# Performance work log

Measured on AMD Instinct MI355X. Metric: run time of the kernel, lower is better.

Reference implementation:

```python
import jax, jax.numpy as jnp
import numpy as np

D = 1024; H = 16; DH = 64; L = 24; S = 4096; DFF = 4096
QB = 7; NC = 2 ** QB; TOPK = 10; EOS = NC + 1
SCALE = float(1.0 / np.sqrt(DH))


def _ln(x, g):
    m = jnp.mean(x, axis=-1, keepdims=True)
    v = jnp.var(x, axis=-1, keepdims=True)
    return (x - m) * jax.lax.rsqrt(v + 1e-5) * g


def _mlp(h, w1, b1, w2, b2, w3, b3):
    h = jax.nn.relu(h @ w1 + b1)
    h = jax.nn.relu(h @ w2 + b2)
    return h @ w3 + b3


def _decode(x, k_cache, v_cache, ln1_g, Wq, Wk, Wv, Wo, ln2_g, Wg, Wu, Wd, lnf_g):
    # single-token decode through L pre-norm layers with KV cache
    def step(h, xs):
        l1, wq, wk, wv, wo, l2, wg, wu, wd, K, V = xs
        hn = _ln(h, l1)
        q = (hn @ wq).reshape(H, DH)
        kn = (hn @ wk).reshape(1, H, DH)
        vn = (hn @ wv).reshape(1, H, DH)
        Kf = jnp.concatenate([K, kn], axis=0)  # [S+1,H,DH]
        Vf = jnp.concatenate([V, vn], axis=0)
        att = jax.nn.softmax(jnp.einsum('hd,shd->hs', q, Kf) * SCALE, axis=-1)
        o = jnp.einsum('hs,shd->hd', att, Vf).reshape(D)
        h = h + o @ wo
        hn = _ln(h, l2)
        h = h + (jax.nn.gelu(hn @ wg) * (hn @ wu)) @ wd  # GLU FF
        return h, None

    res, _ = jax.lax.scan(step, x, (ln1_g, Wq, Wk, Wv, Wo, ln2_g, Wg, Wu, Wd, k_cache, v_cache))
    return _ln(res, lnf_g)


def setup_inputs() -> dict:
    key = jax.random.key(0)
    ks = jax.random.split(key, 40)
    def r(i, shape, s=0.02):
        return jax.random.normal(ks[i], shape, dtype=jnp.float32) * s
    inp = {
        'x': r(0, (D,), 1.0),
        'k_cache': r(1, (L, S, H, DH), 1.0),
        'v_cache': r(2, (L, S, H, DH), 1.0),
        'ln1_g': jnp.ones((L, D), jnp.float32),
        'Wq': r(3, (L, D, D)), 'Wk': r(4, (L, D, D)), 'Wv': r(5, (L, D, D)), 'Wo': r(6, (L, D, D)),
        'ln2_g': jnp.ones((L, D), jnp.float32),
        'Wg': r(7, (L, D, DFF)), 'Wu': r(8, (L, D, DFF)), 'Wd': r(9, (L, DFF, D)),
        'lnf_g': jnp.ones((D,), jnp.float32),
        'h1_w1': r(10, (D, D)), 'h1_b1': jnp.zeros((D,), jnp.float32),
        'h1_w2': r(11, (D, D)), 'h1_b2': jnp.zeros((D,), jnp.float32),
        'h1_w3': r(12, (D, NC + 2)), 'h1_b3': jnp.zeros((NC + 2,), jnp.float32),
        'h2_w1': r(13, (2 * D, D)), 'h2_b1': jnp.zeros((D,), jnp.float32),
        'h2_w2': r(14, (D, D)), 'h2_b2': jnp.zeros((D,), jnp.float32),
        'h2_w3': r(15, (D, NC)), 'h2_b3': jnp.zeros((NC,), jnp.float32),
        'h3_w1': r(16, (3 * D, D)), 'h3_b1': jnp.zeros((D,), jnp.float32),
        'h3_w2': r(17, (D, D)), 'h3_b2': jnp.zeros((D,), jnp.float32),
        'h3_w3': r(18, (D, NC)), 'h3_b3': jnp.zeros((NC,), jnp.float32),
        'c1_emb': r(19, (NC, D), 1.0),
        'c2_emb': r(20, (NC, D), 1.0),
    }
    return inp


def reference(x, k_cache, v_cache, ln1_g, Wq, Wk, Wv, Wo, ln2_g, Wg, Wu, Wd, lnf_g,
              h1_w1, h1_b1, h1_w2, h1_b2, h1_w3, h1_b3,
              h2_w1, h2_b1, h2_w2, h2_b2, h2_w3, h2_b3,
              h3_w1, h3_b1, h3_w2, h3_b2, h3_w3, h3_b3,
              c1_emb, c2_emb):
    res = _decode(x, k_cache, v_cache, ln1_g, Wq, Wk, Wv, Wo, ln2_g, Wg, Wu, Wd, lnf_g)

    k1, k2, k3 = jax.random.split(jax.random.key(42), 3)

    # stage 1: z coordinate (quantized) with EOS-masked top-k sampling
    logits_z = _mlp(res, h1_w1, h1_b1, h1_w2, h1_b2, h1_w3, h1_b3)  # [NC+2]
    tpz, tiz = jax.lax.top_k(jax.nn.softmax(logits_z), TOPK)
    is_eos = tiz[0] == EOS
    mp = tpz * (tiz != EOS).astype(tpz.dtype)
    mp = mp / mp.sum()
    z = jnp.where(is_eos, EOS, tiz[jax.random.categorical(k1, jnp.log(mp + 1e-9))])
    emb_z = c1_emb[jnp.minimum(z, NC - 1)]

    # stage 2: y coordinate
    logits_y = _mlp(jnp.concatenate([res, emb_z]), h2_w1, h2_b1, h2_w2, h2_b2, h2_w3, h2_b3)
    tpy, tiy = jax.lax.top_k(jax.nn.softmax(logits_y), TOPK)
    y = tiy[jax.random.categorical(k2, jnp.log(tpy + 1e-9))]
    emb_y = c2_emb[y]

    # stage 3: x coordinate
    logits_x = _mlp(jnp.concatenate([res, emb_z, emb_y]), h3_w1, h3_b1, h3_w2, h3_b2, h3_w3, h3_b3)
    tpx, tix = jax.lax.top_k(jax.nn.softmax(logits_x), TOPK)
    xc = tix[jax.random.categorical(k3, jnp.log(tpx + 1e-9))]

    xyz = jnp.stack([xc, y, z])
    logits_cat = jnp.concatenate([logits_z, logits_y, logits_x])  # [130+128+128]=386
    return xyz, logits_cat
```

## Files before the change

kernel.cpp:

```cpp
#include <hip/hip_runtime.h>
#include <cstdint>
#include <cstring>
#include <cmath>

constexpr int kH    = 16;
constexpr int kL    = 24;
constexpr int kS    = 4096;
constexpr int kEOS  = 129;
constexpr float kSCALE = 0.125f;
constexpr int kNS   = 32;
constexpr int kTOK  = kS / kNS;

struct G10 { float g[10]; };


__device__ __forceinline__ float wave_sum(float v) {
  v += __shfl_xor(v, 32, 64); v += __shfl_xor(v, 16, 64);
  v += __shfl_xor(v, 8, 64);  v += __shfl_xor(v, 4, 64);
  v += __shfl_xor(v, 2, 64);  v += __shfl_xor(v, 1, 64);
  return v;
}
__device__ __forceinline__ float wave_max(float v) {
  v = fmaxf(v, __shfl_xor(v, 32, 64)); v = fmaxf(v, __shfl_xor(v, 16, 64));
  v = fmaxf(v, __shfl_xor(v, 8, 64));  v = fmaxf(v, __shfl_xor(v, 4, 64));
  v = fmaxf(v, __shfl_xor(v, 2, 64));  v = fmaxf(v, __shfl_xor(v, 1, 64));
  return v;
}
__device__ __forceinline__ float block_sum4(float v, float* red) {
  v = wave_sum(v);
  if ((threadIdx.x & 63) == 0) red[threadIdx.x >> 6] = v;
  __syncthreads();
  float s = red[0] + red[1] + red[2] + red[3];
  __syncthreads();
  return s;
}
__device__ __forceinline__ float block_max4(float v, float* red) {
  v = wave_max(v);
  if ((threadIdx.x & 63) == 0) red[threadIdx.x >> 6] = v;
  __syncthreads();
  float s = fmaxf(fmaxf(red[0], red[1]), fmaxf(red[2], red[3]));
  __syncthreads();
  return s;
}

__device__ __forceinline__ void ln_stats(const float* __restrict__ h, float* red,
                                         float& mean, float& rs) {
  int tid = threadIdx.x;
  float v0 = h[tid], v1 = h[tid + 256], v2 = h[tid + 512], v3 = h[tid + 768];
  float s = block_sum4(v0 + v1 + v2 + v3, red);
  mean = s * (1.0f / 1024.0f);
  float d0 = v0 - mean, d1 = v1 - mean, d2 = v2 - mean, d3 = v3 - mean;
  float sq = block_sum4(d0 * d0 + d1 * d1 + d2 * d2 + d3 * d3, red);
  rs = 1.0f / sqrtf(sq * (1.0f / 1024.0f) + 1e-5f);
}

__device__ __forceinline__ float gelu_f(float x) {
  float t = tanhf(0.7978845608028654f * (x + 0.044715f * x * x * x));
  return 0.5f * x * (1.0f + t);
}


__global__ __launch_bounds__(256) void k_ln_qkv(const float* __restrict__ h,
                                                const float* __restrict__ g,
                                                const float* __restrict__ Wq,
                                                const float* __restrict__ Wk,
                                                const float* __restrict__ Wv,
                                                float* __restrict__ qkv_part,
                                                float* __restrict__ hres) {
  __shared__ float red4[4];
  __shared__ float xs[64];
  __shared__ float4 sh4[256];
  int tid = threadIdx.x;
  float mean, rs;
  ln_stats(h, red4, mean, rs);
  int by = blockIdx.y, rb = by * 64;
  if (tid < 64) xs[tid] = (h[rb + tid] - mean) * rs * g[rb + tid];
  if (blockIdx.x == 0 && tid < 64) hres[rb + tid] = h[rb + tid];
  __syncthreads();
  int c4 = tid & 63, w = tid >> 6;
  int vcol4 = blockIdx.x * 64 + c4;
  int mat = vcol4 >> 8;
  const float* W = (mat == 0) ? Wq : ((mat == 1) ? Wk : Wv);
  const float4* W4 = reinterpret_cast<const float4*>(W);
  int wcol4 = vcol4 & 255;
  float4 acc = {0.f, 0.f, 0.f, 0.f};
  int r0 = w * 16;
  #pragma unroll
  for (int i = 0; i < 16; ++i) {
    int j = r0 + i;
    float xv = xs[j];
    float4 wv = W4[(size_t)(rb + j) * 256 + wcol4];
    acc.x += xv * wv.x; acc.y += xv * wv.y; acc.z += xv * wv.z; acc.w += xv * wv.w;
  }
  sh4[tid] = acc;
  __syncthreads();
  if (tid < 64) {
    float4 a = sh4[tid], b = sh4[tid + 64], c = sh4[tid + 128], d = sh4[tid + 192];
    a.x += b.x + c.x + d.x; a.y += b.y + c.y + d.y;
    a.z += b.z + c.z + d.z; a.w += b.w + c.w + d.w;
    reinterpret_cast<float4*>(qkv_part)[(size_t)by * 768 + blockIdx.x * 64 + tid] = a;
  }
}

__global__ __launch_bounds__(256) void k_attn(const float* __restrict__ qkv_part,
                                              const float* __restrict__ Kc,
                                              const float* __restrict__ Vc,
                                              float* __restrict__ part) {
  __shared__ float4 q4[16];
  __shared__ float4 kn4[16];
  __shared__ float4 vn4[16];
  __shared__ float sc[132];
  __shared__ float red4[4];
  __shared__ float4 ored[16][17];
  int split = blockIdx.x, head = blockIdx.y;
  int tid = threadIdx.x;
  if (tid < 64) {
    float s = 0.f;
    #pragma unroll
    for (int p = 0; p < 16; ++p) s += qkv_part[p * 3072 + head * 64 + tid];
    ((float*)q4)[tid] = s;
  } else if (tid < 128) {
    int d = tid - 64; float s = 0.f;
    #pragma unroll
    for (int p = 0; p < 16; ++p) s += qkv_part[p * 3072 + 1024 + head * 64 + d];
    ((float*)kn4)[d] = s;
  } else if (tid < 192) {
    int d = tid - 128; float s = 0.f;
    #pragma unroll
    for (int p = 0; p < 16; ++p) s += qkv_part[p * 3072 + 2048 + head * 64 + d];
    ((float*)vn4)[d] = s;
  }
  __syncthreads();
  int base = split * kTOK;
  bool last = (split == kNS - 1);
  int count = kTOK + (last ? 1 : 0);
  int wv = tid >> 6, lane = tid & 63, grp = lane >> 4, l16 = lane & 15;
  int g0 = wv * 4 + grp;
  float4 qf = q4[l16];
  const float4* K4 = reinterpret_cast<const float4*>(Kc);
  const float4* V4 = reinterpret_cast<const float4*>(Vc);
  #pragma unroll
  for (int i = 0; i < 8; ++i) {
    int t = g0 + 16 * i;
    float4 kf = K4[(size_t)(base + t) * 256 + head * 16 + l16];
    float d = qf.x * kf.x + qf.y * kf.y + qf.z * kf.z + qf.w * kf.w;
    d += __shfl_xor(d, 1, 16); d += __shfl_xor(d, 2, 16);
    d += __shfl_xor(d, 4, 16); d += __shfl_xor(d, 8, 16);
    if (l16 == 0) sc[t] = d * kSCALE;
  }
  if (last && g0 == 0) {
    float4 kf = kn4[l16];
    float d = qf.x * kf.x + qf.y * kf.y + qf.z * kf.z + qf.w * kf.w;
    d += __shfl_xor(d, 1, 16); d += __shfl_xor(d, 2, 16);
    d += __shfl_xor(d, 4, 16); d += __shfl_xor(d, 8, 16);
    if (l16 == 0) sc[128] = d * kSCALE;
  }
  float4 vreg[8];
  #pragma unroll
  for (int i = 0; i < 8; ++i) {
    int t = g0 + 16 * i;
    vreg[i] = V4[(size_t)(base + t) * 256 + head * 16 + l16];
  }
  __syncthreads();
  float v = (tid < count) ? sc[tid] : -1e30f;
  float m = block_max4(v, red4);
  float pexp = 0.f;
  if (tid < count) { pexp = expf(sc[tid] - m); sc[tid] = pexp; }
  float l = block_sum4(pexp, red4);
  float4 acc = {0.f, 0.f, 0.f, 0.f};
  #pragma unroll
  for (int i = 0; i < 8; ++i) {
    int t = g0 + 16 * i;
    float p = sc[t];
    acc.x += p * vreg[i].x; acc.y += p * vreg[i].y;
    acc.z += p * vreg[i].z; acc.w += p * vreg[i].w;
  }
  if (last && g0 == 0) {
    float p = sc[128];
    float4 vf = vn4[l16];
    acc.x += p * vf.x; acc.y += p * vf.y; acc.z += p * vf.z; acc.w += p * vf.w;
  }
  ored[g0][l16] = acc;
  __syncthreads();
  float* pp = &part[(size_t)(head * kNS + split) * 68];
  if (tid < 16) {
    float4 s = ored[0][tid];
    #pragma unroll
    for (int k = 1; k < 16; ++k) {
      float4 b = ored[k][tid];
      s.x += b.x; s.y += b.y; s.z += b.z; s.w += b.w;
    }
    reinterpret_cast<float4*>(pp + 4)[tid] = s;
  }
  if (tid == 0) { pp[0] = m; pp[1] = l; }
}

__global__ __launch_bounds__(256) void k_comb_wo(const float* __restrict__ part,
                                                 const float* __restrict__ Wo,
                                                 float* __restrict__ hout) {
  __shared__ float o[64];
  __shared__ float4 sh4[256];
  int tid = threadIdx.x;
  int head = blockIdx.y, bx = blockIdx.x;
  if (tid < 64) {
    const float* pp = part + (size_t)(head * kNS) * 68;
    float m = -1e30f;
    for (int s = 0; s < kNS; ++s) m = fmaxf(m, pp[s * 68]);
    float l = 0.f, acc = 0.f;
    for (int s = 0; s < kNS; ++s) {
      float e = expf(pp[s * 68] - m);
      l += e * pp[s * 68 + 1];
      acc += e * pp[s * 68 + 4 + tid];
    }
    o[tid] = acc / l;
  }
  __syncthreads();
  int c4 = tid & 15, w = tid >> 4;
  int vcol4 = bx * 16 + c4;
  const float4* W4 = reinterpret_cast<const float4*>(Wo);
  float4 acc = {0.f, 0.f, 0.f, 0.f};
  int r0 = w * 4;
  #pragma unroll
  for (int i = 0; i < 4; ++i) {
    int r = r0 + i;
    float xv = o[r];
    float4 wv = W4[(size_t)(head * 64 + r) * 256 + vcol4];
    acc.x += xv * wv.x; acc.y += xv * wv.y; acc.z += xv * wv.z; acc.w += xv * wv.w;
  }
  sh4[tid] = acc;
  __syncthreads();
  if (tid < 16) {
    float4 a = sh4[tid];
    #pragma unroll
    for (int k = 1; k < 16; ++k) {
      float4 b = sh4[k * 16 + tid];
      a.x += b.x; a.y += b.y; a.z += b.z; a.w += b.w;
    }
    int vcol = (bx * 16 + tid) * 4;
    atomicAdd(&hout[vcol],     a.x);
    atomicAdd(&hout[vcol + 1], a.y);
    atomicAdd(&hout[vcol + 2], a.z);
    atomicAdd(&hout[vcol + 3], a.w);
  }
}

__global__ __launch_bounds__(256) void k_ln_gu(const float* __restrict__ h,
                                               const float* __restrict__ g,
                                               const float* __restrict__ Wg,
                                               const float* __restrict__ Wu,
                                               float* __restrict__ gu_part,
                                               float* __restrict__ hres) {
  __shared__ float red4[4];
  __shared__ float xs[64];
  __shared__ float4 sh4[256];
  int tid = threadIdx.x;
  float mean, rs;
  ln_stats(h, red4, mean, rs);
  int by = blockIdx.y, rb = by * 64;
  if (tid < 64) xs[tid] = (h[rb + tid] - mean) * rs * g[rb + tid];
  if (blockIdx.x == 0 && tid < 64) hres[rb + tid] = h[rb + tid];
  __syncthreads();
  int c4 = tid & 63, w = tid >> 6;
  int vcol4 = blockIdx.x * 64 + c4;
  int mat = vcol4 >> 10;
  const float4* W4 = reinterpret_cast<const float4*>(mat ? Wu : Wg);
  int wcol4 = vcol4 & 1023;
  float4 acc = {0.f, 0.f, 0.f, 0.f};
  int r0 = w * 16;
  #pragma unroll
  for (int i = 0; i < 16; ++i) {
    int j = r0 + i;
    float xv = xs[j];
    float4 wv = W4[(size_t)(rb + j) * 1024 + wcol4];
    acc.x += xv * wv.x; acc.y += xv * wv.y; acc.z += xv * wv.z; acc.w += xv * wv.w;
  }
  sh4[tid] = acc;
  __syncthreads();
  if (tid < 64) {
    float4 a = sh4[tid], b = sh4[tid + 64], c = sh4[tid + 128], d = sh4[tid + 192];
    a.x += b.x + c.x + d.x; a.y += b.y + c.y + d.y;
    a.z += b.z + c.z + d.z; a.w += b.w + c.w + d.w;
    reinterpret_cast<float4*>(gu_part)[(size_t)by * 2048 + blockIdx.x * 64 + tid] = a;
  }
}

__global__ __launch_bounds__(256) void k_act_wd(const float* __restrict__ gu_part,
                                                const float* __restrict__ Wd,
                                                float* __restrict__ hout) {
  __shared__ float xs[64];
  __shared__ float4 sh4[256];
  int tid = threadIdx.x;
  int by = blockIdx.y, rb = by * 64;
  if (tid < 64) {
    float gs = 0.f, us = 0.f;
    #pragma unroll
    for (int p = 0; p < 16; ++p) {
      gs += gu_part[p * 8192 + rb + tid];
      us += gu_part[p * 8192 + 4096 + rb + tid];
    }
    xs[tid] = gelu_f(gs) * us;
  }
  __syncthreads();
  int c4 = tid & 63, w = tid >> 6;
  int vcol4 = blockIdx.x * 64 + c4;
  const float4* W4 = reinterpret_cast<const float4*>(Wd);
  float4 acc = {0.f, 0.f, 0.f, 0.f};
  int r0 = w * 16;
  #pragma unroll
  for (int i = 0; i < 16; ++i) {
    int j = r0 + i;
    float xv = xs[j];
    float4 wv = W4[(size_t)(rb + j) * 256 + vcol4];
    acc.x += xv * wv.x; acc.y += xv * wv.y; acc.z += xv * wv.z; acc.w += xv * wv.w;
  }
  sh4[tid] = acc;
  __syncthreads();
  if (tid < 64) {
    float4 a = sh4[tid], b = sh4[tid + 64], c = sh4[tid + 128], d = sh4[tid + 192];
    a.x += b.x + c.x + d.x; a.y += b.y + c.y + d.y;
    a.z += b.z + c.z + d.z; a.w += b.w + c.w + d.w;
    int vcol = (blockIdx.x * 64 + tid) * 4;
    atomicAdd(&hout[vcol],     a.x);
    atomicAdd(&hout[vcol + 1], a.y);
    atomicAdd(&hout[vcol + 2], a.z);
    atomicAdd(&hout[vcol + 3], a.w);
  }
}


__global__ __launch_bounds__(256) void k_head_g1(const float* __restrict__ hA,
                                                 const float* __restrict__ lnfg,
                                                 const float* __restrict__ catE,
                                                 const float* __restrict__ W,
                                                 float* __restrict__ t1_part,
                                                 const float* __restrict__ b3,
                                                 float* __restrict__ logits, int n3) {
  __shared__ float red4[4];
  __shared__ float xs[64];
  __shared__ float4 sh4[256];
  int tid = threadIdx.x;
  float mean, rs;
  ln_stats(hA, red4, mean, rs);
  int by = blockIdx.y, rb = by * 64;
  if (blockIdx.x == 0 && by == 0 && tid < n3) logits[tid] = b3[tid];
  if (tid < 64) {
    int r = rb + tid;
    xs[tid] = (r < 1024) ? (hA[r] - mean) * rs * lnfg[r] : catE[r - 1024];
  }
  __syncthreads();
  int c4 = tid & 15, w = tid >> 4;
  int vcol4 = blockIdx.x * 16 + c4;
  const float4* W4 = reinterpret_cast<const float4*>(W);
  float4 acc = {0.f, 0.f, 0.f, 0.f};
  int r0 = w * 4;
  #pragma unroll
  for (int i = 0; i < 4; ++i) {
    float xv = xs[r0 + i];
    float4 wv = W4[(size_t)(rb + r0 + i) * 256 + vcol4];
    acc.x += xv * wv.x; acc.y += xv * wv.y; acc.z += xv * wv.z; acc.w += xv * wv.w;
  }
  sh4[tid] = acc;
  __syncthreads();
  if (tid < 16) {
    float4 a = sh4[tid];
    #pragma unroll
    for (int k = 1; k < 16; ++k) {
      float4 b = sh4[k * 16 + tid];
      a.x += b.x; a.y += b.y; a.z += b.z; a.w += b.w;
    }
    reinterpret_cast<float4*>(t1_part)[(size_t)by * 256 + blockIdx.x * 16 + tid] = a;
  }
}

__global__ __launch_bounds__(256) void k_head_g2(const float* __restrict__ t1_part,
                                                 int ny,
                                                 const float* __restrict__ b1,
                                                 const float* __restrict__ W,
                                                 float* __restrict__ t2_part) {
  __shared__ float xs[64];
  __shared__ float4 sh4[256];
  int tid = threadIdx.x;
  int by = blockIdx.y, rb = by * 64;
  if (tid < 64) {
    float s = b1[rb + tid];
    for (int p = 0; p < ny; ++p) s += t1_part[p * 1024 + rb + tid];
    xs[tid] = fmaxf(s, 0.f);
  }
  __syncthreads();
  int c4 = tid & 15, w = tid >> 4;
  int vcol4 = blockIdx.x * 16 + c4;
  const float4* W4 = reinterpret_cast<const float4*>(W);
  float4 acc = {0.f, 0.f, 0.f, 0.f};
  int r0 = w * 4;
  #pragma unroll
  for (int i = 0; i < 4; ++i) {
    float xv = xs[r0 + i];
    float4 wv = W4[(size_t)(rb + r0 + i) * 256 + vcol4];
    acc.x += xv * wv.x; acc.y += xv * wv.y; acc.z += xv * wv.z; acc.w += xv * wv.w;
  }
  sh4[tid] = acc;
  __syncthreads();
  if (tid < 16) {
    float4 a = sh4[tid];
    #pragma unroll
    for (int k = 1; k < 16; ++k) {
      float4 b = sh4[k * 16 + tid];
      a.x += b.x; a.y += b.y; a.z += b.z; a.w += b.w;
    }
    reinterpret_cast<float4*>(t2_part)[(size_t)by * 256 + blockIdx.x * 16 + tid] = a;
  }
}

__global__ __launch_bounds__(256) void k_head_g3(const float* __restrict__ t2_part,
                                                 const float* __restrict__ b2,
                                                 const float* __restrict__ W,
                                                 float* __restrict__ logits, int n3) {
  __shared__ float xs[64];
  int tid = threadIdx.x;
  int rb = blockIdx.x * 64;
  if (tid < 64) {
    float s = b2[rb + tid];
    #pragma unroll
    for (int p = 0; p < 16; ++p) s += t2_part[p * 1024 + rb + tid];
    xs[tid] = fmaxf(s, 0.f);
  }
  __syncthreads();
  if (tid < n3) {
    float acc = 0.f;
    for (int i = 0; i < 64; ++i) acc += xs[i] * W[(size_t)(rb + i) * n3 + tid];
    atomicAdd(&logits[tid], acc);
  }
}


__global__ void k_sample1(const float* __restrict__ logits,
                          const float* __restrict__ c1_emb,
                          float* __restrict__ embdst,
                          float* __restrict__ out_xyz,
                          G10 gb) {
  __shared__ int zsh;
  int tid = threadIdx.x;
  if (tid == 0) {
    float p[130];
    float mx = -1e30f;
    for (int i = 0; i < 130; ++i) mx = fmaxf(mx, logits[i]);
    float s = 0.f;
    for (int i = 0; i < 130; ++i) { p[i] = expf(logits[i] - mx); s += p[i]; }
    for (int i = 0; i < 130; ++i) p[i] /= s;
    float tp[10]; int ti[10];
    for (int k = 0; k < 10; ++k) {
      float best = -1.f; int bi = 0;
      for (int i = 0; i < 130; ++i)
        if (p[i] > best) { best = p[i]; bi = i; }
      tp[k] = best; ti[k] = bi; p[bi] = -2.f;
    }
    int is_eos = (ti[0] == kEOS);
    float mp[10]; float ssum = 0.f;
    for (int k = 0; k < 10; ++k) {
      mp[k] = tp[k] * ((ti[k] != kEOS) ? 1.f : 0.f);
      ssum += mp[k];
    }
    float bestsc = -1e30f; int ba = 0;
    for (int k = 0; k < 10; ++k) {
      float sc = logf(mp[k] / ssum + 1e-9f) + gb.g[k];
      if (sc > bestsc) { bestsc = sc; ba = k; }
    }
    int z = is_eos ? kEOS : ti[ba];
    zsh = z;
    out_xyz[2] = (float)z;
  }
  __syncthreads();
  int zi = zsh; if (zi > 127) zi = 127;
  for (int i = tid; i < 1024; i += blockDim.x)
    embdst[i] = c1_emb[(size_t)zi * 1024 + i];
}

__global__ void k_sample23(const float* __restrict__ logits,
                           const float* __restrict__ emb,
                           float* __restrict__ embdst,
                           float* __restrict__ outslot,
                           G10 gb) {
  __shared__ int ysh;
  int tid = threadIdx.x;
  if (tid == 0) {
    float p[128];
    float mx = -1e30f;
    for (int i = 0; i < 128; ++i) mx = fmaxf(mx, logits[i]);
    float s = 0.f;
    for (int i = 0; i < 128; ++i) { p[i] = expf(logits[i] - mx); s += p[i]; }
    for (int i = 0; i < 128; ++i) p[i] /= s;
    float tp[10]; int ti[10];
    for (int k = 0; k < 10; ++k) {
      float best = -1.f; int bi = 0;
      for (int i = 0; i < 128; ++i)
        if (p[i] > best) { best = p[i]; bi = i; }
      tp[k] = best; ti[k] = bi; p[bi] = -2.f;
    }
    float bestsc = -1e30f; int ba = 0;
    for (int k = 0; k < 10; ++k) {
      float sc = logf(tp[k] + 1e-9f) + gb.g[k];
      if (sc > bestsc) { bestsc = sc; ba = k; }
    }
    int y = ti[ba];
    ysh = y;
    *outslot = (float)y;
  }
  __syncthreads();
  if (emb != nullptr) {
    int y = ysh;
    for (int i = tid; i < 1024; i += blockDim.x)
      embdst[i] = emb[(size_t)y * 1024 + i];
  }
}


static inline uint32_t rotl32(uint32_t x, uint32_t r) { return (x << r) | (x >> (32 - r)); }

static void threefry2x32(uint32_t k0, uint32_t k1, uint32_t x0, uint32_t x1,
                         uint32_t* o0, uint32_t* o1) {
  uint32_t ks0 = k0, ks1 = k1, ks2 = k0 ^ k1 ^ 0x1BD11BDAu;
  const uint32_t R0[4] = {13, 15, 26, 6};
  const uint32_t R1[4] = {17, 29, 16, 24};
  x0 += ks0; x1 += ks1;
  for (int j = 0; j < 4; ++j) { x0 += x1; x1 = rotl32(x1, R0[j]); x1 ^= x0; }
  x0 += ks1; x1 += ks2 + 1u;
  for (int j = 0; j < 4; ++j) { x0 += x1; x1 = rotl32(x1, R1[j]); x1 ^= x0; }
  x0 += ks2; x1 += ks0 + 2u;
  for (int j = 0; j < 4; ++j) { x0 += x1; x1 = rotl32(x1, R0[j]); x1 ^= x0; }
  x0 += ks0; x1 += ks1 + 3u;
  for (int j = 0; j < 4; ++j) { x0 += x1; x1 = rotl32(x1, R1[j]); x1 ^= x0; }
  x0 += ks1; x1 += ks2 + 4u;
  for (int j = 0; j < 4; ++j) { x0 += x1; x1 = rotl32(x1, R0[j]); x1 ^= x0; }
  x0 += ks2; x1 += ks0 + 5u;
  *o0 = x0; *o1 = x1;
}

static void gumbel10_part(uint32_t k0, uint32_t k1, float* g) {
  const float tiny = 1.1754943508222875e-38f;
  for (int i = 0; i < 10; ++i) {
    uint32_t a, c;
    threefry2x32(k0, k1, 0u, (uint32_t)i, &a, &c);
    uint32_t bits = a ^ c;
    uint32_t fb = (bits >> 9) | 0x3f800000u;
    float f; memcpy(&f, &fb, 4);
    f -= 1.0f;
    float u = f * (1.0f - tiny) + tiny;
    if (u < tiny) u = tiny;
    g[i] = -logf(-logf(u));
  }
}


extern "C" void kernel_launch(void* const* d_in, const int* in_sizes, int n_in,
                              void* d_out, int out_size, void* d_ws, size_t ws_size,
                              hipStream_t stream) {
  (void)in_sizes; (void)n_in; (void)out_size; (void)ws_size;
  const float* x      = (const float*)d_in[0];
  const float* kcache = (const float*)d_in[1];
  const float* vcache = (const float*)d_in[2];
  const float* ln1g   = (const float*)d_in[3];
  const float* Wq     = (const float*)d_in[4];
  const float* Wk     = (const float*)d_in[5];
  const float* Wv     = (const float*)d_in[6];
  const float* Wo     = (const float*)d_in[7];
  const float* ln2g   = (const float*)d_in[8];
  const float* Wg     = (const float*)d_in[9];
  const float* Wu     = (const float*)d_in[10];
  const float* Wd     = (const float*)d_in[11];
  const float* lnfg   = (const float*)d_in[12];
  const float* h1w1 = (const float*)d_in[13]; const float* h1b1 = (const float*)d_in[14];
  const float* h1w2 = (const float*)d_in[15]; const float* h1b2 = (const float*)d_in[16];
  const float* h1w3 = (const float*)d_in[17]; const float* h1b3 = (const float*)d_in[18];
  const float* h2w1 = (const float*)d_in[19]; const float* h2b1 = (const float*)d_in[20];
  const float* h2w2 = (const float*)d_in[21]; const float* h2b2 = (const float*)d_in[22];
  const float* h2w3 = (const float*)d_in[23]; const float* h2b3 = (const float*)d_in[24];
  const float* h3w1 = (const float*)d_in[25]; const float* h3b1 = (const float*)d_in[26];
  const float* h3w2 = (const float*)d_in[27]; const float* h3b2 = (const float*)d_in[28];
  const float* h3w3 = (const float*)d_in[29]; const float* h3b3 = (const float*)d_in[30];
  const float* c1emb = (const float*)d_in[31];
  const float* c2emb = (const float*)d_in[32];

  float* ws = (float*)d_ws;
  float* hA   = ws;
  float* hB   = ws + 1024;
  float* qkvp = ws + 2048;
  float* part = ws + 51200;
  float* gup  = ws + 86016;
  float* catE = ws + 217088;
  float* t2p  = ws + 219136;
  float* t1p  = gup;
  float* out  = (float*)d_out;

  for (int l = 0; l < kL; ++l) {
    const float* Wq_l = Wq + (size_t)l * 1024 * 1024;
    const float* Wk_l = Wk + (size_t)l * 1024 * 1024;
    const float* Wv_l = Wv + (size_t)l * 1024 * 1024;
    const float* Wo_l = Wo + (size_t)l * 1024 * 1024;
    const float* Wg_l = Wg + (size_t)l * 1024 * 4096;
    const float* Wu_l = Wu + (size_t)l * 1024 * 4096;
    const float* Wd_l = Wd + (size_t)l * 4096 * 1024;
    const float* Kc_l = kcache + (size_t)l * kS * 1024;
    const float* Vc_l = vcache + (size_t)l * kS * 1024;
    const float* h_in = (l == 0) ? x : hA;

    k_ln_qkv<<<dim3(12, 16), 256, 0, stream>>>(h_in, ln1g + (size_t)l * 1024,
                                               Wq_l, Wk_l, Wv_l, qkvp, hB);
    k_attn<<<dim3(kNS, kH), 256, 0, stream>>>(qkvp, Kc_l, Vc_l, part);
    k_comb_wo<<<dim3(16, kH), 256, 0, stream>>>(part, Wo_l, hB);
    k_ln_gu<<<dim3(32, 16), 256, 0, stream>>>(hB, ln2g + (size_t)l * 1024,
                                              Wg_l, Wu_l, gup, hA);
    k_act_wd<<<dim3(4, 64), 256, 0, stream>>>(gup, Wd_l, hA);
  }

  uint32_t k1a, k1b, k2a, k2b, k3a, k3b;
  threefry2x32(0u, 42u, 0u, 0u, &k1a, &k1b);
  threefry2x32(0u, 42u, 0u, 1u, &k2a, &k2b);
  threefry2x32(0u, 42u, 0u, 2u, &k3a, &k3b);
  G10 G1, G2, G3;
  gumbel10_part(k1a, k1b, G1.g);
  gumbel10_part(k2a, k2b, G2.g);
  gumbel10_part(k3a, k3b, G3.g);

  k_head_g1<<<dim3(16, 16), 256, 0, stream>>>(hA, lnfg, catE, h1w1, t1p, h1b3, out + 3, 130);
  k_head_g2<<<dim3(16, 16), 256, 0, stream>>>(t1p, 16, h1b1, h1w2, t2p);
  k_head_g3<<<16, 256, 0, stream>>>(t2p, h1b2, h1w3, out + 3, 130);
  k_sample1<<<1, 256, 0, stream>>>(out + 3, c1emb, catE, out, G1);

  k_head_g1<<<dim3(16, 32), 256, 0, stream>>>(hA, lnfg, catE, h2w1, t1p, h2b3, out + 133, 128);
  k_head_g2<<<dim3(16, 16), 256, 0, stream>>>(t1p, 32, h2b1, h2w2, t2p);
  k_head_g3<<<16, 256, 0, stream>>>(t2p, h2b2, h2w3, out + 133, 128);
  k_sample23<<<1, 256, 0, stream>>>(out + 133, c2emb, catE + 1024, out + 1, G2);

  k_head_g1<<<dim3(16, 48), 256, 0, stream>>>(hA, lnfg, catE, h3w1, t1p, h3b3, out + 261, 128);
  k_head_g2<<<dim3(16, 16), 256, 0, stream>>>(t1p, 48, h3b1, h3w2, t2p);
  k_head_g3<<<16, 256, 0, stream>>>(t2p, h3b2, h3w3, out + 261, 128);
  k_sample23<<<1, 256, 0, stream>>>(out + 261, nullptr, nullptr, out + 0, G3);
}
```

Before: 1.241 ms.

## Fuse top-k sampling into head GEMV blocks and widen QKV grid

The single-threaded sampling kernels are replaced by a wave-parallel softmax/top-k sampler. That sampler is recomputed redundantly inside each head first-layer block that needs the sampled embedding, which removes two kernel launches and the serial 130-element loops. Separately, the QKV projection grid grows from 12 to 48 column blocks with 16 row-groups per block, to raise occupancy for the memory-bound GEMV. The trade-off is redundant sampler work in many blocks and a longer in-block reduction over 16 partials.

New measurement: 1.138 ms, median of 2. 8.3% less time.

```diff
diff --git a/kernel.cpp b/kernel.cpp
--- a/kernel.cpp
+++ b/kernel.cpp
@@ -57,6 +57,65 @@
 __device__ __forceinline__ float gelu_f(float x) {
   float t = tanhf(0.7978845608028654f * (x + 0.044715f * x * x * x));
   return 0.5f * x * (1.0f + t);
+}
+
+__device__ int wave_sampler(const float* __restrict__ logits, int n3,
+                            const float* __restrict__ gb, bool eosmode,
+                            int* ish) {
+  int tid = threadIdx.x;
+  if (tid < 64) {
+    float a0 = (tid < n3) ? logits[tid] : -1e30f;
+    float a1 = (tid + 64 < n3) ? logits[tid + 64] : -1e30f;
+    float a2 = (tid + 128 < n3) ? logits[tid + 128] : -1e30f;
+    float m = wave_max(fmaxf(a0, fmaxf(a1, a2)));
+    float p0 = expf(a0 - m), p1 = expf(a1 - m), p2 = expf(a2 - m);
+    float s = wave_sum(p0 + p1 + p2);
+    p0 = p0 / s; p1 = p1 / s; p2 = p2 / s;
+    float tp[10]; int ti[10];
+    #pragma unroll
+    for (int k = 0; k < 10; ++k) {
+      float bv = p0; int bi = tid;
+      if (p1 > bv) { bv = p1; bi = tid + 64; }
+      if (p2 > bv) { bv = p2; bi = tid + 128; }
+      #pragma unroll
+      for (int off = 32; off > 0; off >>= 1) {
+        float ov = __shfl_xor(bv, off, 64);
+        int   oi = __shfl_xor(bi, off, 64);
+        if (ov > bv || (ov == bv && oi < bi)) { bv = ov; bi = oi; }
+      }
+      tp[k] = bv; ti[k] = bi;
+      if (bi == tid) p0 = -2.f;
+      else if (bi == tid + 64) p1 = -2.f;
+      else if (bi == tid + 128) p2 = -2.f;
+    }
+    if (tid == 0) {
+      int choice;
+      if (eosmode) {
+        int is_eos = (ti[0] == kEOS);
+        float mp[10]; float msum = 0.f;
+        for (int k = 0; k < 10; ++k) {
+          mp[k] = tp[k] * ((ti[k] != kEOS) ? 1.f : 0.f);
+          msum += mp[k];
+        }
+        float bestsc = -1e30f; int ba = 0;
+        for (int k = 0; k < 10; ++k) {
+          float sc = logf(mp[k] / msum + 1e-9f) + gb[k];
+          if (sc > bestsc) { bestsc = sc; ba = k; }
+        }
+        choice = is_eos ? kEOS : ti[ba];
+      } else {
+        float bestsc = -1e30f; int ba = 0;
+        for (int k = 0; k < 10; ++k) {
+          float sc = logf(tp[k] + 1e-9f) + gb[k];
+          if (sc > bestsc) { bestsc = sc; ba = k; }
+        }
+        choice = ti[ba];
+      }
+      *ish = choice;
+    }
+  }
+  __syncthreads();
+  return *ish;
 }
 
 
@@ -77,16 +136,16 @@
   if (tid < 64) xs[tid] = (h[rb + tid] - mean) * rs * g[rb + tid];
   if (blockIdx.x == 0 && tid < 64) hres[rb + tid] = h[rb + tid];
   __syncthreads();
-  int c4 = tid & 63, w = tid >> 6;
-  int vcol4 = blockIdx.x * 64 + c4;
+  int c4 = tid & 15, w = tid >> 4;
+  int vcol4 = blockIdx.x * 16 + c4;
   int mat = vcol4 >> 8;
   const float* W = (mat == 0) ? Wq : ((mat == 1) ? Wk : Wv);
   const float4* W4 = reinterpret_cast<const float4*>(W);
   int wcol4 = vcol4 & 255;
   float4 acc = {0.f, 0.f, 0.f, 0.f};
-  int r0 = w * 16;
-  #pragma unroll
-  for (int i = 0; i < 16; ++i) {
+  int r0 = w * 4;
+  #pragma unroll
+  for (int i = 0; i < 4; ++i) {
     int j = r0 + i;
     float xv = xs[j];
     float4 wv = W4[(size_t)(rb + j) * 256 + wcol4];
@@ -94,11 +153,14 @@
   }
   sh4[tid] = acc;
   __syncthreads();
-  if (tid < 64) {
-    float4 a = sh4[tid], b = sh4[tid + 64], c = sh4[tid + 128], d = sh4[tid + 192];
-    a.x += b.x + c.x + d.x; a.y += b.y + c.y + d.y;
-    a.z += b.z + c.z + d.z; a.w += b.w + c.w + d.w;
-    reinterpret_cast<float4*>(qkv_part)[(size_t)by * 768 + blockIdx.x * 64 + tid] = a;
+  if (tid < 16) {
+    float4 a = sh4[tid];
+    #pragma unroll
+    for (int k = 1; k < 16; ++k) {
+      float4 b = sh4[k * 16 + tid];
+      a.x += b.x; a.y += b.y; a.z += b.z; a.w += b.w;
+    }
+    reinterpret_cast<float4*>(qkv_part)[(size_t)by * 768 + blockIdx.x * 16 + tid] = a;
   }
 }
 
@@ -330,22 +392,44 @@
 
 __global__ __launch_bounds__(256) void k_head_g1(const float* __restrict__ hA,
                                                  const float* __restrict__ lnfg,
-                                                 const float* __restrict__ catE,
+                                                 const float* __restrict__ c1emb,
+                                                 const float* __restrict__ c2emb,
+                                                 const float* __restrict__ zlogits,
+                                                 const float* __restrict__ ylogits,
+                                                 G10 Gz, G10 Gy,
                                                  const float* __restrict__ W,
                                                  float* __restrict__ t1_part,
                                                  const float* __restrict__ b3,
-                                                 float* __restrict__ logits, int n3) {
+                                                 float* __restrict__ logits, int n3,
+                                                 float* __restrict__ outz,
+                                                 float* __restrict__ outy) {
   __shared__ float red4[4];
   __shared__ float xs[64];
   __shared__ float4 sh4[256];
-  int tid = threadIdx.x;
+  __shared__ int ish;
+  int tid = threadIdx.x;
+  int by = blockIdx.y, rb = by * 64;
+  int zv = 0, yv = 0;
+  if (by >= 16 && by < 32) {
+    zv = wave_sampler(zlogits, 130, Gz.g, true, &ish);
+    if (outz && blockIdx.x == 0 && by == 16 && tid == 0) *outz = (float)zv;
+  } else if (by >= 32) {
+    yv = wave_sampler(ylogits, 128, Gy.g, false, &ish);
+    if (outy && blockIdx.x == 0 && by == 32 && tid == 0) *outy = (float)yv;
+  }
   float mean, rs;
   ln_stats(hA, red4, mean, rs);
-  int by = blockIdx.y, rb = by * 64;
   if (blockIdx.x == 0 && by == 0 && tid < n3) logits[tid] = b3[tid];
   if (tid < 64) {
     int r = rb + tid;
-    xs[tid] = (r < 1024) ? (hA[r] - mean) * rs * lnfg[r] : catE[r - 1024];
+    if (r < 1024) {
+      xs[tid] = (hA[r] - mean) * rs * lnfg[r];
+    } else if (r < 2048) {
+      int zi = zv > 127 ? 127 : zv;
+      xs[tid] = c1emb[(size_t)zi * 1024 + (r - 1024)];
+    } else {
+      xs[tid] = c2emb[(size_t)yv * 1024 + (r - 2048)];
+    }
   }
   __syncthreads();
   int c4 = tid & 15, w = tid >> 4;
@@ -432,85 +516,11 @@
   }
 }
 
-
-__global__ void k_sample1(const float* __restrict__ logits,
-                          const float* __restrict__ c1_emb,
-                          float* __restrict__ embdst,
-                          float* __restrict__ out_xyz,
-                          G10 gb) {
-  __shared__ int zsh;
-  int tid = threadIdx.x;
-  if (tid == 0) {
-    float p[130];
-    float mx = -1e30f;
-    for (int i = 0; i < 130; ++i) mx = fmaxf(mx, logits[i]);
-    float s = 0.f;
-    for (int i = 0; i < 130; ++i) { p[i] = expf(logits[i] - mx); s += p[i]; }
-    for (int i = 0; i < 130; ++i) p[i] /= s;
-    float tp[10]; int ti[10];
-    for (int k = 0; k < 10; ++k) {
-      float best = -1.f; int bi = 0;
-      for (int i = 0; i < 130; ++i)
-        if (p[i] > best) { best = p[i]; bi = i; }
-      tp[k] = best; ti[k] = bi; p[bi] = -2.f;
-    }
-    int is_eos = (ti[0] == kEOS);
-    float mp[10]; float ssum = 0.f;
-    for (int k = 0; k < 10; ++k) {
-      mp[k] = tp[k] * ((ti[k] != kEOS) ? 1.f : 0.f);
-      ssum += mp[k];
-    }
-    float bestsc = -1e30f; int ba = 0;
-    for (int k = 0; k < 10; ++k) {
-      float sc = logf(mp[k] / ssum + 1e-9f) + gb.g[k];
-      if (sc > bestsc) { bestsc = sc; ba = k; }
-    }
-    int z = is_eos ? kEOS : ti[ba];
-    zsh = z;
-    out_xyz[2] = (float)z;
-  }
-  __syncthreads();
-  int zi = zsh; if (zi > 127) zi = 127;
-  for (int i = tid; i < 1024; i += blockDim.x)
-    embdst[i] = c1_emb[(size_t)zi * 1024 + i];
-}
-
-__global__ void k_sample23(const float* __restrict__ logits,
-                           const float* __restrict__ emb,
-                           float* __restrict__ embdst,
-                           float* __restrict__ outslot,
-                           G10 gb) {
-  __shared__ int ysh;
-  int tid = threadIdx.x;
-  if (tid == 0) {
-    float p[128];
-    float mx = -1e30f;
-    for (int i = 0; i < 128; ++i) mx = fmaxf(mx, logits[i]);
-    float s = 0.f;
-    for (int i = 0; i < 128; ++i) { p[i] = expf(logits[i] - mx); s += p[i]; }
-    for (int i = 0; i < 128; ++i) p[i] /= s;
-    float tp[10]; int ti[10];
-    for (int k = 0; k < 10; ++k) {
-      float best = -1.f; int bi = 0;
-      for (int i = 0; i < 128; ++i)
-        if (p[i] > best) { best = p[i]; bi = i; }
-      tp[k] = best; ti[k] = bi; p[bi] = -2.f;
-    }
-    float bestsc = -1e30f; int ba = 0;
-    for (int k = 0; k < 10; ++k) {
-      float sc = logf(tp[k] + 1e-9f) + gb.g[k];
-      if (sc > bestsc) { bestsc = sc; ba = k; }
-    }
-    int y = ti[ba];
-    ysh = y;
-    *outslot = (float)y;
-  }
-  __syncthreads();
-  if (emb != nullptr) {
-    int y = ysh;
-    for (int i = tid; i < 1024; i += blockDim.x)
-      embdst[i] = emb[(size_t)y * 1024 + i];
-  }
+__global__ void k_sample_final(const float* __restrict__ logits,
+                               float* __restrict__ outslot, G10 gb) {
+  __shared__ int ish;
+  int v = wave_sampler(logits, 128, gb.g, false, &ish);
+  if (threadIdx.x == 0) *outslot = (float)v;
 }
 
 
@@ -586,8 +596,7 @@
   float* qkvp = ws + 2048;
   float* part = ws + 51200;
   float* gup  = ws + 86016;
-  float* catE = ws + 217088;
-  float* t2p  = ws + 219136;
+  float* t2p  = ws + 217088;
   float* t1p  = gup;
   float* out  = (float*)d_out;
 
@@ -603,7 +612,7 @@
     const float* Vc_l = vcache + (size_t)l * kS * 1024;
     const float* h_in = (l == 0) ? x : hA;
 
-    k_ln_qkv<<<dim3(12, 16), 256, 0, stream>>>(h_in, ln1g + (size_t)l * 1024,
+    k_ln_qkv<<<dim3(48, 16), 256, 0, stream>>>(h_in, ln1g + (size_t)l * 1024,
                                                Wq_l, Wk_l, Wv_l, qkvp, hB);
     k_attn<<<dim3(kNS, kH), 256, 0, stream>>>(qkvp, Kc_l, Vc_l, part);
     k_comb_wo<<<dim3(16, kH), 256, 0, stream>>>(part, Wo_l, hB);
@@ -616,23 +625,35 @@
   threefry2x32(0u, 42u, 0u, 0u, &k1a, &k1b);
   threefry2x32(0u, 42u, 0u, 1u, &k2a, &k2b);
   threefry2x32(0u, 42u, 0u, 2u, &k3a, &k3b);
-  G10 G1, G2, G3;
+  G10 G1, G2, G3, G0;
   gumbel10_part(k1a, k1b, G1.g);
   gumbel10_part(k2a, k2b, G2.g);
   gumbel10_part(k3a, k3b, G3.g);
-
-  k_head_g1<<<dim3(16, 16), 256, 0, stream>>>(hA, lnfg, catE, h1w1, t1p, h1b3, out + 3, 130);
+  memset(G0.g, 0, sizeof(G0.g));
+
+  float* logz = out + 3;
+  float* logy = out + 133;
+  float* logx = out + 261;
+
+  k_head_g1<<<dim3(16, 16), 256, 0, stream>>>(hA, lnfg, c1emb, c2emb,
+                                              nullptr, nullptr, G0, G0,
+                                              h1w1, t1p, h1b3, logz, 130,
+                                              nullptr, nullptr);
   k_head_g2<<<dim3(16, 16), 256, 0, stream>>>(t1p, 16, h1b1, h1w2, t2p);
-  k_head_g3<<<16, 256, 0, stream>>>(t2p, h1b2, h1w3, out + 3, 130);
-  k_sample1<<<1, 256, 0, stream>>>(out + 3, c1emb, catE, out, G1);
-
-  k_head_g1<<<dim3(16, 32), 256, 0, stream>>>(hA, lnfg, catE, h2w1, t1p, h2b3, out + 133, 128);
+  k_head_g3<<<16, 256, 0, stream>>>(t2p, h1b2, h1w3, logz, 130);
+
+  k_head_g1<<<dim3(16, 32), 256, 0, stream>>>(hA, lnfg, c1emb, c2emb,
+                                              logz, nullptr, G1, G0,
+                                              h2w1, t1p, h2b3, logy, 128,
+                                              out + 2, nullptr);
   k_head_g2<<<dim3(16, 16), 256, 0, stream>>>(t1p, 32, h2b1, h2w2, t2p);
-  k_head_g3<<<16, 256, 0, stream>>>(t2p, h2b2, h2w3, out + 133, 128);
-  k_sample23<<<1, 256, 0, stream>>>(out + 133, c2emb, catE + 1024, out + 1, G2);
-
-  k_head_g1<<<dim3(16, 48), 256, 0, stream>>>(hA, lnfg, catE, h3w1, t1p, h3b3, out + 261, 128);
+  k_head_g3<<<16, 256, 0, stream>>>(t2p, h2b2, h2w3, logy, 128);
+
+  k_head_g1<<<dim3(16, 48), 256, 0, stream>>>(hA, lnfg, c1emb, c2emb,
+                                              logz, logy, G1, G2,
+                                              h3w1, t1p, h3b3, logx, 128,
+                                              nullptr, out + 1);
   k_head_g2<<<dim3(16, 16), 256, 0, stream>>>(t1p, 48, h3b1, h3w2, t2p);
-  k_head_g3<<<16, 256, 0, stream>>>(t2p, h3b2, h3w3, out + 261, 128);
-  k_sample23<<<1, 256, 0, stream>>>(out + 261, nullptr, nullptr, out + 0, G3);
-}
+  k_head_g3<<<16, 256, 0, stream>>>(t2p, h3b2, h3w3, logx, 128);
+  k_sample_final<<<1, 256, 0, stream>>>(logx, out + 0, G3);
+}
```
